# Kernel optimization log

Measured on AMD Instinct MI355X. Metric: run time of the kernel, lower is better.

The kernel has to match this reference:

```python
import jax, jax.numpy as jnp
import numpy as np

WS = 16            # window size (patch grid)
NP = WS * WS       # 256 patch tokens
N = NP + 1         # +1 CLS
H = 16             # heads
LN_EPS = 1e-5


def _rel_pos_index():
    ch, cw = np.meshgrid(np.arange(WS), np.arange(WS), indexing='ij')
    flat = np.stack([ch.reshape(-1), cw.reshape(-1)])            # [2, NP]
    rel = flat[:, :, None] - flat[:, None, :]                    # [2, NP, NP]
    rel = rel.transpose(1, 2, 0).astype(np.int64)                # [NP, NP, 2]
    rel[:, :, 0] += WS - 1
    rel[:, :, 1] += WS - 1
    rel[:, :, 0] *= 2 * WS - 1
    nrd = (2 * WS - 1) * (2 * WS - 1) + 3                        # 964
    idx = np.zeros((N, N), dtype=np.int64)
    idx[1:, 1:] = rel.sum(-1)
    idx[0, 0:] = nrd - 3
    idx[0:, 0] = nrd - 2
    idx[0, 0] = nrd - 1
    return idx

REL_IDX = _rel_pos_index()


def layernorm(x, g, b):
    mu = x.mean(-1, keepdims=True)
    var = x.var(-1, keepdims=True)
    return (x - mu) * jax.lax.rsqrt(var + LN_EPS) * g + b


def rotate_half(t):
    t1, t2 = t[..., ::2], t[..., 1::2]
    return jnp.stack([-t2, t1], axis=-1).reshape(t.shape)


def apply_rope(t, cos, sin):
    # t: [B, H, NP, hd]; cos/sin: [NP, hd]
    return t * cos + rotate_half(t) * sin


def setup_inputs() -> dict:
    key = jax.random.key(0)
    ks = jax.random.split(key, 20)
    D, Hd = 1024, 4096
    s = lambda d: 1.0 / np.sqrt(d)
    return {
        'x': jax.random.normal(ks[0], (64, N, D), jnp.float32),
        'rope_cos': jnp.cos(jnp.arange(NP)[:, None] * jnp.exp(-jnp.arange(64) / 16.0)[None, :]),
        'rope_sin': jnp.sin(jnp.arange(NP)[:, None] * jnp.exp(-jnp.arange(64) / 16.0)[None, :]),
        'q_w': jax.random.normal(ks[1], (D, D)) * s(D),
        'q_b': jnp.zeros((D,)),
        'k_w': jax.random.normal(ks[2], (D, D)) * s(D),
        'v_w': jax.random.normal(ks[3], (D, D)) * s(D),
        'v_b': jnp.zeros((D,)),
        'rel_bias_table': jax.random.normal(ks[4], (964, H)) * 0.02,
        'inner_ln_g': jnp.ones((D,)), 'inner_ln_b': jnp.zeros((D,)),
        'proj_w': jax.random.normal(ks[5], (D, D)) * s(D),
        'proj_b': jnp.zeros((D,)),
        'norm1_g': jnp.ones((D,)), 'norm1_b': jnp.zeros((D,)),
        'norm2_g': jnp.ones((D,)), 'norm2_b': jnp.zeros((D,)),
        'w1_w': jax.random.normal(ks[6], (Hd, D)) * s(D),
        'w1_b': jnp.zeros((Hd,)),
        'w2_w': jax.random.normal(ks[7], (Hd, D)) * s(D),
        'w2_b': jnp.zeros((Hd,)),
        'ffn_ln_g': jnp.ones((Hd,)), 'ffn_ln_b': jnp.zeros((Hd,)),
        'w3_w': jax.random.normal(ks[8], (D, Hd)) * s(Hd),
        'w3_b': jnp.zeros((D,)),
    }


def reference(x, rope_cos, rope_sin, q_w, q_b, k_w, v_w, v_b, rel_bias_table,
              inner_ln_g, inner_ln_b, proj_w, proj_b, norm1_g, norm1_b,
              norm2_g, norm2_b, w1_w, w1_b, w2_w, w2_b, ffn_ln_g, ffn_ln_b,
              w3_w, w3_b):
    B, Ntok, D = x.shape
    hd = D // H
    scale = hd ** -0.5

    # ---- attention branch (pre-norm, subln path) ----
    xn = layernorm(x, norm1_g, norm1_b)
    q = (xn @ q_w.T + q_b).reshape(B, Ntok, H, hd).transpose(0, 2, 1, 3)
    k = (xn @ k_w.T).reshape(B, Ntok, H, hd).transpose(0, 2, 1, 3)
    v = (xn @ v_w.T + v_b).reshape(B, Ntok, H, hd).transpose(0, 2, 1, 3)

    # RoPE on all tokens except CLS
    q = jnp.concatenate([q[:, :, :1], apply_rope(q[:, :, 1:], rope_cos, rope_sin)], axis=2)
    k = jnp.concatenate([k[:, :, :1], apply_rope(k[:, :, 1:], rope_cos, rope_sin)], axis=2)

    attn = jnp.einsum('bhqd,bhkd->bhqk', q * scale, k)
    # relative position bias: [N, N, H] -> [H, N, N]
    rel_bias = rel_bias_table[REL_IDX.reshape(-1)].reshape(Ntok, Ntok, H).transpose(2, 0, 1)
    attn = attn + rel_bias[None]
    attn = jax.nn.softmax(attn, axis=-1)

    out = jnp.einsum('bhqk,bhkd->bqhd', attn, v).reshape(B, Ntok, D)
    out = layernorm(out, inner_ln_g, inner_ln_b)     # inner_attn_ln (subln)
    out = out @ proj_w.T + proj_b
    x = x + out

    # ---- SwiGLU MLP branch ----
    xn2 = layernorm(x, norm2_g, norm2_b)
    x1 = xn2 @ w1_w.T + w1_b
    x2 = xn2 @ w2_w.T + w2_b
    hidden = jax.nn.silu(x1) * x2
    hidden = layernorm(hidden, ffn_ln_g, ffn_ln_b)   # ffn_ln (subln)
    x = x + (hidden @ w3_w.T + w3_b)
    return x
```

## Files before the change

kernel.cpp:

```cpp
#include <hip/hip_runtime.h>
#include <stdint.h>

typedef __bf16 bf16;
typedef __attribute__((ext_vector_type(8))) __bf16 bf16x8;
typedef __attribute__((ext_vector_type(4))) float floatx4;

__device__ inline float bflo(uint32_t u){ union{uint32_t v; float f;} t; t.v = u << 16; return t.f; }
__device__ inline float bfhi(uint32_t u){ union{uint32_t v; float f;} t; t.v = u & 0xffff0000u; return t.f; }
__device__ inline uint32_t pack2(float a, float b){ union{ bf16 h[2]; uint32_t u; } t; t.h[0]=(bf16)a; t.h[1]=(bf16)b; return t.u; }

__device__ inline void load4(const bf16* p, float* x){
  uint2 u = *(const uint2*)p; x[0]=bflo(u.x); x[1]=bfhi(u.x); x[2]=bflo(u.y); x[3]=bfhi(u.y);
}
__device__ inline void load4(const float* p, float* x){
  float4 u = *(const float4*)p; x[0]=u.x; x[1]=u.y; x[2]=u.z; x[3]=u.w;
}

__device__ inline void gload16(const void* g, void* l){
  __builtin_amdgcn_global_load_lds((const __attribute__((address_space(1))) uint32_t*)g,
                                   (__attribute__((address_space(3))) uint32_t*)l, 16, 0, 0);
}

__global__ __launch_bounds__(256) void cvt_kernel(const float* __restrict__ in, bf16* __restrict__ out,
                                                  int n8, float scale)
{
  int i = blockIdx.x * 256 + threadIdx.x;
  if (i >= n8) return;
  const float* p = in + (size_t)i * 8;
  float4 a = *(const float4*)p;
  float4 b = *(const float4*)(p + 4);
  union{ uint4 q; bf16 h[8]; } pk;
  pk.h[0]=(bf16)(a.x*scale); pk.h[1]=(bf16)(a.y*scale); pk.h[2]=(bf16)(a.z*scale); pk.h[3]=(bf16)(a.w*scale);
  pk.h[4]=(bf16)(b.x*scale); pk.h[5]=(bf16)(b.y*scale); pk.h[6]=(bf16)(b.z*scale); pk.h[7]=(bf16)(b.w*scale);
  *(uint4*)(out + (size_t)i*8) = pk.q;
}

__global__ __launch_bounds__(256) void qkvb_fill(const float* __restrict__ qb, const float* __restrict__ vb,
                                                 float* __restrict__ out)
{
  int i = blockIdx.x * 256 + threadIdx.x;
  float v = 0.f;
  if (i < 1024) v = qb[i] * 0.125f;
  else if (i >= 2048) v = vb[i - 2048];
  out[i] = v;
}

__global__ __launch_bounds__(256) void bias_fill(const float* __restrict__ tab, bf16* __restrict__ biasB)
{
  int t = blockIdx.x * 256 + threadIdx.x;
  if (t >= 16*272*272) return;
  int kg = t % 272;
  int rem = t / 272;
  int qg = rem % 272;
  int h = rem / 272;
  float v;
  if (kg > 256) v = -3e38f;
  else {
    int qq = min(qg, 256);
    int idx;
    if (qq == 0 && kg == 0) idx = 963;
    else if (qq == 0) idx = 961;
    else if (kg == 0) idx = 962;
    else { int p = qq - 1, pk = kg - 1;
           idx = ((p >> 4) - (pk >> 4) + 15) * 31 + ((p & 15) - (pk & 15) + 15); }
    v = tab[idx*16 + h];
  }
  biasB[t] = (bf16)v;
}

template<int W, typename TIN>
__global__ __launch_bounds__(256) void ln_kernel(const TIN* in, const float* __restrict__ g,
                                                 const float* __restrict__ bb, bf16* out, int M)
{
  constexpr int E = W / 256;
  int row = blockIdx.x; if (row >= M) return;
  int tid = threadIdx.x;
  const TIN* rp = in + (size_t)row * W + tid * E;
  float x[E];
  #pragma unroll
  for (int j = 0; j < E; j += 4) load4(rp + j, &x[j]);
  float s = 0.f, ss = 0.f;
  #pragma unroll
  for (int e = 0; e < E; e++){ s += x[e]; ss += x[e]*x[e]; }
  #pragma unroll
  for (int k = 32; k >= 1; k >>= 1){ s += __shfl_xor(s, k, 64); ss += __shfl_xor(ss, k, 64); }
  __shared__ float rs_[4], rq_[4];
  if ((tid & 63) == 0){ rs_[tid >> 6] = s; rq_[tid >> 6] = ss; }
  __syncthreads();
  s = rs_[0]+rs_[1]+rs_[2]+rs_[3]; ss = rq_[0]+rq_[1]+rq_[2]+rq_[3];
  float mean = s * (1.0f / W);
  float var  = ss * (1.0f / W) - mean * mean;
  float rinv = rsqrtf(var + 1e-5f);
  bf16* op = out + (size_t)row * W + tid * E;
  const float* gp = g + tid * E;
  const float* bp = bb + tid * E;
  #pragma unroll
  for (int j = 0; j < E; j += 4){
    float gv[4], bv[4];
    load4(gp + j, gv); load4(bp + j, bv);
    float y0 = (x[j]  -mean)*rinv*gv[0] + bv[0];
    float y1 = (x[j+1]-mean)*rinv*gv[1] + bv[1];
    float y2 = (x[j+2]-mean)*rinv*gv[2] + bv[2];
    float y3 = (x[j+3]-mean)*rinv*gv[3] + bv[3];
    uint2 o; o.x = pack2(y0, y1); o.y = pack2(y2, y3);
    *(uint2*)(op + j) = o;
  }
}

template<typename TE, typename TC>
__global__ __launch_bounds__(256) void gemm_bt(const bf16* __restrict__ A, const bf16* __restrict__ Bw,
                                               const float* __restrict__ bias, const TE* extra,
                                               TC* C, int M, int N, int K, int mode)
{
  __shared__ __align__(16) bf16 As[128*32];
  __shared__ __align__(16) bf16 Bs[128*32];
  int tid = threadIdx.x;
  int lane = tid & 63, wave = tid >> 6;
  int l16 = lane & 15, quad = lane >> 4;
  int wm = wave >> 1, wn = wave & 1;
  int m0 = blockIdx.y * 128, n0 = blockIdx.x * 128;
  floatx4 acc[4][4];
  #pragma unroll
  for (int i = 0; i < 4; i++)
    #pragma unroll
    for (int j = 0; j < 4; j++) acc[i][j] = (floatx4){0.f,0.f,0.f,0.f};
  int nk = K >> 5;
  int rowS = tid >> 2;
  int colS = (tid & 3) * 8;
  int ra0 = min(m0 + rowS,      M-1);
  int ra1 = min(m0 + 64 + rowS, M-1);
  int rb0 = min(n0 + rowS,      N-1);
  int rb1 = min(n0 + 64 + rowS, N-1);
  const bf16* pa0 = A  + (size_t)ra0 * K + colS;
  const bf16* pa1 = A  + (size_t)ra1 * K + colS;
  const bf16* pb0 = Bw + (size_t)rb0 * K + colS;
  const bf16* pb1 = Bw + (size_t)rb1 * K + colS;
  bf16* la0 = &As[tid*8];        bf16* la1 = &As[2048 + tid*8];
  bf16* lb0 = &Bs[tid*8];        bf16* lb1 = &Bs[2048 + tid*8];
  auto stage = [&](int kt){
    int ko = kt * 32;
    gload16(pa0 + ko, la0);
    gload16(pa1 + ko, la1);
    gload16(pb0 + ko, lb0);
    gload16(pb1 + ko, lb1);
  };
  stage(0);
  int kt = 0;
  while (true){
    __syncthreads();
    bf16x8 af[4], bfv[4];
    #pragma unroll
    for (int i = 0; i < 4; i++) af[i]  = *(const bf16x8*)&As[(wm*64 + i*16 + l16)*32 + quad*8];
    #pragma unroll
    for (int j = 0; j < 4; j++) bfv[j] = *(const bf16x8*)&Bs[(wn*64 + j*16 + l16)*32 + quad*8];
    ++kt;
    bool more = kt < nk;
    if (more){
      __syncthreads();
      stage(kt);
    }
    #pragma unroll
    for (int i = 0; i < 4; i++)
      #pragma unroll
      for (int j = 0; j < 4; j++)
        acc[i][j] = __builtin_amdgcn_mfma_f32_16x16x32_bf16(af[i], bfv[j], acc[i][j], 0, 0, 0);
    if (!more) break;
  }
  #pragma unroll
  for (int i = 0; i < 4; i++){
    int gmb = m0 + wm*64 + i*16 + quad*4;
    #pragma unroll
    for (int j = 0; j < 4; j++){
      int gn = n0 + wn*64 + j*16 + l16;
      float bv = bias ? bias[gn] : 0.f;
      #pragma unroll
      for (int r = 0; r < 4; r++){
        int gm = gmb + r;
        if (gm < M){
          float v = acc[i][j][r] + bv;
          if (mode == 1) v += (float)extra[(size_t)gm * N + gn];
          else if (mode == 2){ float a = (float)extra[(size_t)gm * N + gn]; v *= a / (1.f + __expf(-a)); }
          C[(size_t)gm * N + gn] = (TC)v;
        }
      }
    }
  }
}

template<typename TE, typename TC>
__global__ __launch_bounds__(512) void gemm256(const bf16* __restrict__ A, const bf16* __restrict__ Bw,
                                               const float* __restrict__ bias, const TE* extra,
                                               TC* C, int M, int N, int K, int mode)
{
  __shared__ __align__(16) bf16 lds[65536];
  int tid = threadIdx.x;
  int lane = tid & 63, wave = tid >> 6;
  int l16 = lane & 15, quad = lane >> 4;
  int wm = wave >> 2, wn = wave & 3;

  int nwg = gridDim.x * gridDim.y;
  int orig = blockIdx.y * gridDim.x + blockIdx.x;
  int qq = nwg >> 3, rr = nwg & 7;
  int xcd = orig & 7, idx = orig >> 3;
  int wg = (xcd < rr ? xcd*(qq+1) : rr*(qq+1) + (xcd-rr)*qq) + idx;
  int bx = wg % gridDim.x, by = wg / gridDim.x;
  int m0 = by * 256, n0 = bx * 256;

  floatx4 acc[8][4];
  #pragma unroll
  for (int i = 0; i < 8; i++)
    #pragma unroll
    for (int j = 0; j < 4; j++) acc[i][j] = (floatx4){0.f,0.f,0.f,0.f};
  int nk = K >> 6;

  int srow = tid >> 3, sseg = tid & 7;
  int sA = ((sseg ^ (srow & 7)) << 3);
  const bf16* pA[4]; const bf16* pB[4];
  #pragma unroll
  for (int jj = 0; jj < 4; jj++){
    pA[jj] = A  + (size_t)min(m0 + jj*64 + srow, M-1) * K + sA;
    pB[jj] = Bw + (size_t)min(n0 + jj*64 + srow, N-1) * K + sA;
  }
  auto stage = [&](int kt, int b){
    int ko = kt * 64;
    bf16* as = lds + (b ? 16384 : 0);
    bf16* bs = lds + 32768 + (b ? 16384 : 0);
    #pragma unroll
    for (int jj = 0; jj < 4; jj++){
      gload16(pA[jj] + ko, as + jj*4096 + tid*8);
      gload16(pB[jj] + ko, bs + jj*4096 + tid*8);
    }
  };

  stage(0, 0);
  int cur = 0;
  for (int kt = 0; kt < nk; ++kt){
    bool more = (kt + 1) < nk;
    if (more){
      stage(kt + 1, cur ^ 1);
      asm volatile("s_waitcnt vmcnt(8)" ::: "memory");
    } else {
      asm volatile("s_waitcnt vmcnt(0)" ::: "memory");
    }
    __builtin_amdgcn_s_barrier();
    asm volatile("" ::: "memory");
    bf16* as = lds + (cur ? 16384 : 0);
    bf16* bs = lds + 32768 + (cur ? 16384 : 0);
    #pragma unroll
    for (int kk = 0; kk < 2; kk++){
      bf16x8 af[8], bfv[4];
      #pragma unroll
      for (int i = 0; i < 8; i++){
        int r = wm*128 + i*16 + l16;
        af[i] = *(const bf16x8*)&as[r*64 + (((kk*4 + quad) ^ (l16 & 7)) << 3)];
      }
      #pragma unroll
      for (int j = 0; j < 4; j++){
        int c = wn*64 + j*16 + l16;
        bfv[j] = *(const bf16x8*)&bs[c*64 + (((kk*4 + quad) ^ (l16 & 7)) << 3)];
      }
      __builtin_amdgcn_s_setprio(1);
      #pragma unroll
      for (int i = 0; i < 8; i++)
        #pragma unroll
        for (int j = 0; j < 4; j++)
          acc[i][j] = __builtin_amdgcn_mfma_f32_16x16x32_bf16(af[i], bfv[j], acc[i][j], 0, 0, 0);
      __builtin_amdgcn_s_setprio(0);
    }
    asm volatile("" ::: "memory");
    __builtin_amdgcn_s_barrier();
    cur ^= 1;
  }

  #pragma unroll
  for (int i = 0; i < 8; i++){
    int gmb = m0 + wm*128 + i*16 + quad*4;
    #pragma unroll
    for (int j = 0; j < 4; j++){
      int gn = n0 + wn*64 + j*16 + l16;
      float bv = bias ? bias[gn] : 0.f;
      #pragma unroll
      for (int r = 0; r < 4; r++){
        int gm = gmb + r;
        if (gm < M){
          float v = acc[i][j][r] + bv;
          if (mode == 1) v += (float)extra[(size_t)gm * N + gn];
          else if (mode == 2){ float a = (float)extra[(size_t)gm * N + gn]; v *= a / (1.f + __expf(-a)); }
          C[(size_t)gm * N + gn] = (TC)v;
        }
      }
    }
  }
}

__global__ __launch_bounds__(256) void rope_kernel(bf16* __restrict__ qkv,
                                                   const float* __restrict__ cs, const float* __restrict__ sn)
{
  uint32_t i = blockIdx.x * 256u + threadIdx.x;
  int d0 = (int)(i & 511) * 2;
  int tok = (int)((i >> 9) & 255);
  int b = (int)(i >> 17);
  int j = d0 & 63;
  float c0 = cs[tok*64 + j], c1 = cs[tok*64 + j + 1];
  float s0 = sn[tok*64 + j], s1 = sn[tok*64 + j + 1];
  size_t off = ((size_t)(b*257 + tok + 1)) * 3072 + d0;
  uint32_t uq = *(const uint32_t*)(qkv + off);
  float x0 = bflo(uq), x1 = bfhi(uq);
  *(uint32_t*)(qkv + off) = pack2(x0*c0 - x1*s0, x1*c1 + x0*s1);
  uint32_t uk = *(const uint32_t*)(qkv + off + 1024);
  float y0 = bflo(uk), y1 = bfhi(uk);
  *(uint32_t*)(qkv + off + 1024) = pack2(y0*c0 - y1*s0, y1*c1 + y0*s1);
}

__global__ __launch_bounds__(256, 2) void attn_kernel(const bf16* __restrict__ QKV,
                                                      const bf16* __restrict__ biasB,
                                                      bf16* __restrict__ AO)
{
  constexpr int VS = 280;
  __shared__ __align__(16) bf16 Ks[272*64];
  __shared__ __align__(16) bf16 Vt[64*VS];
  __shared__ __align__(16) bf16 Os[4][16*72];
  int id = blockIdx.x;
  int h = id & 15, b = id >> 4;
  int tid = threadIdx.x, lane = tid & 63, wave = tid >> 6;
  int l16 = lane & 15, quad = lane >> 4;
  size_t baseQ = (size_t)(b*257) * 3072 + h*64;
  const bf16* Kg = QKV + baseQ + 1024;
  const bf16* Vg = QKV + baseQ + 2048;
  size_t aoBase = (size_t)(b*257) * 1024 + h*64;

  for (int i = tid; i < 272*8; i += 256){
    int row = i >> 3, seg = i & 7;
    int tok = min(row, 256);
    gload16(Kg + (size_t)tok*3072 + ((seg ^ (row & 7)) * 8), &Ks[i*8]);
  }
  for (int i = tid; i < 272*8; i += 256){
    int row = i >> 3, seg = i & 7;
    int tok = min(row, 256);
    uint4 v = *(const uint4*)(Vg + (size_t)tok*3072 + seg*8);
    uint4 w;
    w.x = (uint32_t)__shfl_xor((int)v.x, 8, 64);
    w.y = (uint32_t)__shfl_xor((int)v.y, 8, 64);
    w.z = (uint32_t)__shfl_xor((int)v.z, 8, 64);
    w.w = (uint32_t)__shfl_xor((int)v.w, 8, 64);
    union { uint4 q4; bf16 h8[8]; } mv, pv; mv.q4 = v; pv.q4 = w;
    int rb = row & ~1;
    if ((row & 1) == 0){
      #pragma unroll
      for (int jj = 0; jj < 4; jj++){
        union { uint32_t u; bf16 hh[2]; } pk; pk.hh[0] = mv.h8[jj]; pk.hh[1] = pv.h8[jj];
        *(uint32_t*)&Vt[(seg*8 + jj)*VS + rb] = pk.u;
      }
    } else {
      #pragma unroll
      for (int jj = 4; jj < 8; jj++){
        union { uint32_t u; bf16 hh[2]; } pk; pk.hh[0] = pv.h8[jj]; pk.hh[1] = mv.h8[jj];
        *(uint32_t*)&Vt[(seg*8 + jj)*VS + rb] = pk.u;
      }
    }
  }
  __syncthreads();

  int srcA = l16 + 16*((2*quad)     & 3);
  int srcB = l16 + 16*((2*quad + 1) & 3);

  for (int qt = wave; qt < 17; qt += 4){
    int q0 = qt * 16;
    int qrow = min(q0 + l16, 256);
    const bf16* qp = QKV + baseQ + (size_t)qrow*3072;
    bf16x8 qb0 = *(const bf16x8*)(qp + quad*8);
    bf16x8 qb1 = *(const bf16x8*)(qp + 32 + quad*8);

    const bf16* bp = biasB + ((size_t)(h*272) + (q0 + l16)) * 272;
    uint2 bu[17];
    #pragma unroll
    for (int nt = 0; nt < 17; nt++) bu[nt] = *(const uint2*)(bp + nt*16 + quad*4);

    floatx4 S[17];
    #pragma unroll
    for (int nt = 0; nt < 17; nt++){
      int row = nt*16 + l16;
      bf16x8 ka0 = *(const bf16x8*)&Ks[row*64 + ((quad     ^ (l16 & 7)) * 8)];
      bf16x8 ka1 = *(const bf16x8*)&Ks[row*64 + (((4+quad) ^ (l16 & 7)) * 8)];
      floatx4 c = (floatx4){0.f,0.f,0.f,0.f};
      c = __builtin_amdgcn_mfma_f32_16x16x32_bf16(ka0, qb0, c, 0, 0, 0);
      c = __builtin_amdgcn_mfma_f32_16x16x32_bf16(ka1, qb1, c, 0, 0, 0);
      S[nt] = c;
    }

    float m = -3e38f;
    #pragma unroll
    for (int nt = 0; nt < 17; nt++){
      S[nt][0] += bflo(bu[nt].x); S[nt][1] += bfhi(bu[nt].x);
      S[nt][2] += bflo(bu[nt].y); S[nt][3] += bfhi(bu[nt].y);
      m = fmaxf(m, fmaxf(fmaxf(S[nt][0], S[nt][1]), fmaxf(S[nt][2], S[nt][3])));
    }
    m = fmaxf(m, __shfl_xor(m, 16, 64));
    m = fmaxf(m, __shfl_xor(m, 32, 64));

    float lsum = 0.f;
    uint32_t pklo[17], pkhi[17];
    #pragma unroll
    for (int nt = 0; nt < 17; nt++){
      float p0 = __expf(S[nt][0] - m), p1 = __expf(S[nt][1] - m);
      float p2 = __expf(S[nt][2] - m), p3 = __expf(S[nt][3] - m);
      lsum += (p0 + p1) + (p2 + p3);
      pklo[nt] = pack2(p0, p1); pkhi[nt] = pack2(p2, p3);
    }
    lsum += __shfl_xor(lsum, 16, 64);
    lsum += __shfl_xor(lsum, 32, 64);

    floatx4 o[4];
    #pragma unroll
    for (int dt = 0; dt < 4; dt++) o[dt] = (floatx4){0.f,0.f,0.f,0.f};
    #pragma unroll
    for (int ks = 0; ks < 9; ks++){
      uint32_t t0[4], t1[4];
      t0[0] = (uint32_t)__shfl((int)pklo[2*ks], srcA, 64);
      t0[1] = (uint32_t)__shfl((int)pkhi[2*ks], srcA, 64);
      t0[2] = (uint32_t)__shfl((int)pklo[2*ks], srcB, 64);
      t0[3] = (uint32_t)__shfl((int)pkhi[2*ks], srcB, 64);
      if (2*ks + 1 <= 16){
        t1[0] = (uint32_t)__shfl((int)pklo[2*ks+1], srcA, 64);
        t1[1] = (uint32_t)__shfl((int)pkhi[2*ks+1], srcA, 64);
        t1[2] = (uint32_t)__shfl((int)pklo[2*ks+1], srcB, 64);
        t1[3] = (uint32_t)__shfl((int)pkhi[2*ks+1], srcB, 64);
      } else {
        t1[0] = 0; t1[1] = 0; t1[2] = 0; t1[3] = 0;
      }
      union { uint32_t u[4]; bf16x8 v; } pa;
      bool lowhalf = (quad < 2);
      pa.u[0] = lowhalf ? t0[0] : t1[0];
      pa.u[1] = lowhalf ? t0[1] : t1[1];
      pa.u[2] = lowhalf ? t0[2] : t1[2];
      pa.u[3] = lowhalf ? t0[3] : t1[3];
      #pragma unroll
      for (int dt = 0; dt < 4; dt++){
        bf16x8 vb = *(const bf16x8*)&Vt[(dt*16 + l16)*VS + ks*32 + quad*8];
        o[dt] = __builtin_amdgcn_mfma_f32_16x16x32_bf16(pa.v, vb, o[dt], 0, 0, 0);
      }
    }

    #pragma unroll
    for (int r = 0; r < 4; r++){
      int qr = quad*4 + r;
      float ls = __shfl(lsum, qr, 64);
      float rinv = 1.0f / ls;
      #pragma unroll
      for (int dt = 0; dt < 4; dt++)
        Os[wave][qr*72 + dt*16 + l16] = (bf16)(o[dt][r] * rinv);
    }
    #pragma unroll
    for (int half = 0; half < 2; half++){
      int rowL = (lane >> 3) + half*8;
      int chunk = lane & 7;
      int q = q0 + rowL;
      uint4 ov = *(const uint4*)&Os[wave][rowL*72 + chunk*8];
      if (q <= 256) *(uint4*)&AO[aoBase + (size_t)q*1024 + chunk*8] = ov;
    }
  }
}

extern "C" void kernel_launch(void* const* d_in, const int* in_sizes, int n_in,
                              void* d_out, int out_size, void* d_ws, size_t ws_size,
                              hipStream_t stream)
{
  (void)in_sizes; (void)n_in; (void)out_size; (void)ws_size;
  const float* x    = (const float*)d_in[0];
  const float* rc   = (const float*)d_in[1];
  const float* rsn  = (const float*)d_in[2];
  const float* q_w  = (const float*)d_in[3];
  const float* q_b  = (const float*)d_in[4];
  const float* k_w  = (const float*)d_in[5];
  const float* v_w  = (const float*)d_in[6];
  const float* v_b  = (const float*)d_in[7];
  const float* tab  = (const float*)d_in[8];
  const float* ig   = (const float*)d_in[9];
  const float* ib   = (const float*)d_in[10];
  const float* pw   = (const float*)d_in[11];
  const float* pb   = (const float*)d_in[12];
  const float* n1g  = (const float*)d_in[13];
  const float* n1b  = (const float*)d_in[14];
  const float* n2g  = (const float*)d_in[15];
  const float* n2b  = (const float*)d_in[16];
  const float* w1w  = (const float*)d_in[17];
  const float* w1b  = (const float*)d_in[18];
  const float* w2w  = (const float*)d_in[19];
  const float* w2b  = (const float*)d_in[20];
  const float* fg   = (const float*)d_in[21];
  const float* fb   = (const float*)d_in[22];
  const float* w3w  = (const float*)d_in[23];
  const float* w3b  = (const float*)d_in[24];

  const int M = 64 * 257;
  const int D = 1024, HD = 4096;
  char* ws = (char*)d_ws;
  const size_t CHB = (size_t)M * D * 2;
  bf16* B0 = (bf16*)(ws);
  bf16* B1 = (bf16*)(ws + CHB);
  bf16* B2 = (bf16*)(ws + 2*CHB);
  bf16* B3 = (bf16*)(ws + 3*CHB);
  bf16* WQ = (bf16*)(ws + 4*CHB);
  bf16* WK = WQ + (size_t)D*D;
  bf16* WV = WK + (size_t)D*D;
  bf16* WP = WV + (size_t)D*D;
  bf16* W1 = WP + (size_t)D*D;
  bf16* W2 = W1 + (size_t)HD*D;
  bf16* W3 = W2 + (size_t)HD*D;
  float* QKVB = (float*)(W3 + (size_t)HD*D);
  bf16* XN  = B0;
  bf16* QKV = B1;
  bf16* AO  = B0;
  bf16* AOL = B1;
  bf16* X1  = B2;
  bf16* XN2 = B3;
  bf16* HS  = B0;
  bf16* biasB = (bf16*)d_out;
  float* OUT = (float*)d_out;

  dim3 blk(256), blk2(512);
  dim3 g1(D/128, (M + 127)/128);
  dim3 gqkv(3072/256, (M + 255)/256);

  const int n8_D = D*D/8;
  const int n8_H = HD*D/8;
  cvt_kernel<<<dim3(n8_D/256), blk, 0, stream>>>(q_w, WQ, n8_D, 0.125f);
  cvt_kernel<<<dim3(n8_D/256), blk, 0, stream>>>(k_w, WK, n8_D, 1.f);
  cvt_kernel<<<dim3(n8_D/256), blk, 0, stream>>>(v_w, WV, n8_D, 1.f);
  cvt_kernel<<<dim3(n8_D/256), blk, 0, stream>>>(pw,  WP, n8_D, 1.f);
  cvt_kernel<<<dim3(n8_H/256), blk, 0, stream>>>(w1w, W1, n8_H, 1.f);
  cvt_kernel<<<dim3(n8_H/256), blk, 0, stream>>>(w2w, W2, n8_H, 1.f);
  cvt_kernel<<<dim3(n8_H/256), blk, 0, stream>>>(w3w, W3, n8_H, 1.f);
  qkvb_fill<<<dim3(12), blk, 0, stream>>>(q_b, v_b, QKVB);
  bias_fill<<<dim3((16*272*272 + 255)/256), blk, 0, stream>>>(tab, biasB);

  ln_kernel<1024, float><<<dim3(M), blk, 0, stream>>>(x, n1g, n1b, XN, M);
  gemm256<bf16, bf16><<<gqkv, blk2, 0, stream>>>(XN, WQ, QKVB, (const bf16*)nullptr, QKV, M, 3072, D, 0);
  rope_kernel<<<dim3(64*256*512/256), blk, 0, stream>>>(QKV, rc, rsn);
  attn_kernel<<<dim3(64*16), blk, 0, stream>>>(QKV, biasB, AO);
  ln_kernel<1024, bf16><<<dim3(M), blk, 0, stream>>>(AO, ig, ib, AOL, M);
  gemm_bt<float, bf16><<<g1, blk, 0, stream>>>(AOL, WP, pb, x, X1, M, D, D, 1);
  ln_kernel<1024, bf16><<<dim3(M), blk, 0, stream>>>(X1, n2g, n2b, XN2, M);

  const int MC = M / 2;
  dim3 g2(HD/256, (MC + 255)/256);
  dim3 g1c(D/128, (MC + 127)/128);
  for (int c = 0; c < 2; c++){
    const bf16* a2 = XN2 + (size_t)c * MC * D;
    const bf16* x1 = X1  + (size_t)c * MC * D;
    float*      oc = OUT + (size_t)c * MC * D;
    gemm256<bf16, bf16><<<g2, blk2, 0, stream>>>(a2, W1, w1b, (const bf16*)nullptr, HS, MC, HD, D, 0);
    gemm256<bf16, bf16><<<g2, blk2, 0, stream>>>(a2, W2, w2b, HS, HS, MC, HD, D, 2);
    ln_kernel<4096, bf16><<<dim3(MC), blk, 0, stream>>>(HS, fg, fb, HS, MC);
    gemm_bt<bf16, float><<<g1c, blk, 0, stream>>>(HS, W3, w3b, x1, oc, MC, D, HD, 1);
  }
}
```

Before: 1.857 ms.

## Interleave next-tile global loads with MFMA phases in 256x256 GEMM

Restructures the GEMM main loop into four compute phases per K-tile. The next tile's global-to-LDS loads are issued in two halves during the first two phases, and each phase loads only the A fragments it needs, which spreads memory issue across the MFMA work. It also declares launch bounds with one block per CU and drops one barrier per iteration by waiting only at the end of each tile. B fragments for both k-substeps are held in registers at once, which raises register pressure, and the full vmcnt(0) wait at the end of each tile may expose load latency.

```diff
diff --git a/kernel.cpp b/kernel.cpp
--- a/kernel.cpp
+++ b/kernel.cpp
@@ -188,9 +188,9 @@
 }
 
 template<typename TE, typename TC>
-__global__ __launch_bounds__(512) void gemm256(const bf16* __restrict__ A, const bf16* __restrict__ Bw,
-                                               const float* __restrict__ bias, const TE* extra,
-                                               TC* C, int M, int N, int K, int mode)
+__global__ __launch_bounds__(512, 1) void gemm_pl(const bf16* __restrict__ A, const bf16* __restrict__ Bw,
+                                                  const float* __restrict__ bias, const TE* extra,
+                                                  TC* C, int M, int N, int K, int mode)
 {
   __shared__ __align__(16) bf16 lds[65536];
   int tid = threadIdx.x;
@@ -221,55 +221,62 @@
     pA[jj] = A  + (size_t)min(m0 + jj*64 + srow, M-1) * K + sA;
     pB[jj] = Bw + (size_t)min(n0 + jj*64 + srow, N-1) * K + sA;
   }
-  auto stage = [&](int kt, int b){
+  auto stageH = [&](int kt, int b, int half){
     int ko = kt * 64;
     bf16* as = lds + (b ? 16384 : 0);
     bf16* bs = lds + 32768 + (b ? 16384 : 0);
     #pragma unroll
-    for (int jj = 0; jj < 4; jj++){
+    for (int jj = half*2; jj < half*2 + 2; jj++){
       gload16(pA[jj] + ko, as + jj*4096 + tid*8);
       gload16(pB[jj] + ko, bs + jj*4096 + tid*8);
     }
   };
 
-  stage(0, 0);
-  int cur = 0;
-  for (int kt = 0; kt < nk; ++kt){
-    bool more = (kt + 1) < nk;
-    if (more){
-      stage(kt + 1, cur ^ 1);
-      asm volatile("s_waitcnt vmcnt(8)" ::: "memory");
-    } else {
-      asm volatile("s_waitcnt vmcnt(0)" ::: "memory");
-    }
-    __builtin_amdgcn_s_barrier();
-    asm volatile("" ::: "memory");
-    bf16* as = lds + (cur ? 16384 : 0);
-    bf16* bs = lds + 32768 + (cur ? 16384 : 0);
-    #pragma unroll
-    for (int kk = 0; kk < 2; kk++){
-      bf16x8 af[8], bfv[4];
-      #pragma unroll
-      for (int i = 0; i < 8; i++){
-        int r = wm*128 + i*16 + l16;
-        af[i] = *(const bf16x8*)&as[r*64 + (((kk*4 + quad) ^ (l16 & 7)) << 3)];
-      }
-      #pragma unroll
-      for (int j = 0; j < 4; j++){
-        int c = wn*64 + j*16 + l16;
-        bfv[j] = *(const bf16x8*)&bs[c*64 + (((kk*4 + quad) ^ (l16 & 7)) << 3)];
-      }
-      __builtin_amdgcn_s_setprio(1);
-      #pragma unroll
-      for (int i = 0; i < 8; i++)
+  stageH(0, 0, 0); stageH(0, 0, 1);
+  asm volatile("s_waitcnt vmcnt(0)" ::: "memory");
+  __builtin_amdgcn_s_barrier();
+
+  for (int t = 0; t < nk; ++t){
+    int cur = t & 1;
+    const bf16* as = lds + (cur ? 16384 : 0);
+    const bf16* bs = lds + 32768 + (cur ? 16384 : 0);
+    bool more = (t + 1) < nk;
+    bf16x8 bfv[4][2];
+    #pragma unroll
+    for (int ph = 0; ph < 4; ph++){
+      if (ph < 2 && more) stageH(t + 1, cur ^ 1, ph);
+      if (ph == 0){
         #pragma unroll
         for (int j = 0; j < 4; j++)
-          acc[i][j] = __builtin_amdgcn_mfma_f32_16x16x32_bf16(af[i], bfv[j], acc[i][j], 0, 0, 0);
+          #pragma unroll
+          for (int kk = 0; kk < 2; kk++){
+            int c = wn*64 + j*16 + l16;
+            bfv[j][kk] = *(const bf16x8*)&bs[c*64 + (((kk*4 + quad) ^ (l16 & 7)) << 3)];
+          }
+      }
+      bf16x8 af[2][2];
+      #pragma unroll
+      for (int ii = 0; ii < 2; ii++)
+        #pragma unroll
+        for (int kk = 0; kk < 2; kk++){
+          int r = wm*128 + (ph*2 + ii)*16 + l16;
+          af[ii][kk] = *(const bf16x8*)&as[r*64 + (((kk*4 + quad) ^ (l16 & 7)) << 3)];
+        }
+      __builtin_amdgcn_s_setprio(1);
+      #pragma unroll
+      for (int ii = 0; ii < 2; ii++)
+        #pragma unroll
+        for (int kk = 0; kk < 2; kk++)
+          #pragma unroll
+          for (int j = 0; j < 4; j++)
+            acc[ph*2 + ii][j] = __builtin_amdgcn_mfma_f32_16x16x32_bf16(af[ii][kk], bfv[j][kk],
+                                                                        acc[ph*2 + ii][j], 0, 0, 0);
       __builtin_amdgcn_s_setprio(0);
     }
-    asm volatile("" ::: "memory");
-    __builtin_amdgcn_s_barrier();
-    cur ^= 1;
+    if (more){
+      asm volatile("s_waitcnt vmcnt(0)" ::: "memory");
+      __builtin_amdgcn_s_barrier();
+    }
   }
 
   #pragma unroll
@@ -535,7 +542,7 @@
   bias_fill<<<dim3((16*272*272 + 255)/256), blk, 0, stream>>>(tab, biasB);
 
   ln_kernel<1024, float><<<dim3(M), blk, 0, stream>>>(x, n1g, n1b, XN, M);
-  gemm256<bf16, bf16><<<gqkv, blk2, 0, stream>>>(XN, WQ, QKVB, (const bf16*)nullptr, QKV, M, 3072, D, 0);
+  gemm_pl<bf16, bf16><<<gqkv, blk2, 0, stream>>>(XN, WQ, QKVB, (const bf16*)nullptr, QKV, M, 3072, D, 0);
   rope_kernel<<<dim3(64*256*512/256), blk, 0, stream>>>(QKV, rc, rsn);
   attn_kernel<<<dim3(64*16), blk, 0, stream>>>(QKV, biasB, AO);
   ln_kernel<1024, bf16><<<dim3(M), blk, 0, stream>>>(AO, ig, ib, AOL, M);
@@ -549,8 +556,8 @@
     const bf16* a2 = XN2 + (size_t)c * MC * D;
     const bf16* x1 = X1  + (size_t)c * MC * D;
     float*      oc = OUT + (size_t)c * MC * D;
-    gemm256<bf16, bf16><<<g2, blk2, 0, stream>>>(a2, W1, w1b, (const bf16*)nullptr, HS, MC, HD, D, 0);
-    gemm256<bf16, bf16><<<g2, blk2, 0, stream>>>(a2, W2, w2b, HS, HS, MC, HD, D, 2);
+    gemm_pl<bf16, bf16><<<g2, blk2, 0, stream>>>(a2, W1, w1b, (const bf16*)nullptr, HS, MC, HD, D, 0);
+    gemm_pl<bf16, bf16><<<g2, blk2, 0, stream>>>(a2, W2, w2b, HS, HS, MC, HD, D, 2);
     ln_kernel<4096, bf16><<<dim3(MC), blk, 0, stream>>>(HS, fg, fb, HS, MC);
     gemm_bt<bf16, float><<<g1c, blk, 0, stream>>>(HS, W3, w3b, x1, oc, MC, D, HD, 1);
   }
```

Measured after the change: 1.875 ms. Within noise of the previous version (+1.0%).
